# Performance work log

Measured on AMD Instinct MI355X. Metric: run time of the kernel, lower is better.

The kernel has to match this reference:

```python
import jax, jax.numpy as jnp
import numpy as np

# dims: batch, seq, d_model, heads, blocks
B, S, D, H, L = 8, 2048, 128, 4, 2
DK = D // H
SCALE = 1.0 / float(DK) ** 0.5
EPS = 1e-8  # LayerNorm eps from the torch module
NEG = -1000000000.0


def _ln(x, g, b):
    m = jnp.mean(x, axis=-1, keepdims=True)
    v = jnp.mean((x - m) ** 2, axis=-1, keepdims=True)
    return (x - m) * jax.lax.rsqrt(v + EPS) * g + b


def setup_inputs() -> dict:
    key = jax.random.key(0)
    ks = jax.random.split(key, 16)
    s = 0.02
    return {
        "log_seqs": jax.random.randint(ks[0], (B, S), 0, 50000),
        "seqs": jax.random.normal(ks[1], (B, S, D), dtype=jnp.float32),
        "Wqkv": jax.random.normal(ks[2], (L, 3, D, D), dtype=jnp.float32) * s,
        "bqkv": jnp.zeros((L, 3, D), dtype=jnp.float32),
        "ln1_g": jnp.ones((L, D), dtype=jnp.float32),
        "ln1_b": jnp.zeros((L, D), dtype=jnp.float32),
        "ln2_g": jnp.ones((L, D), dtype=jnp.float32),
        "ln2_b": jnp.zeros((L, D), dtype=jnp.float32),
        "W1": jax.random.normal(ks[3], (L, D, D), dtype=jnp.float32) * s,
        "b1": jnp.zeros((L, D), dtype=jnp.float32),
        "W2": jax.random.normal(ks[4], (L, D, D), dtype=jnp.float32) * s,
        "b2": jnp.zeros((L, D), dtype=jnp.float32),
        "lng": jnp.ones((D,), dtype=jnp.float32),
        "lnb": jnp.zeros((D,), dtype=jnp.float32),
    }


def reference(log_seqs, seqs, Wqkv, bqkv, ln1_g, ln1_b, ln2_g, ln2_b,
              W1, b1, W2, b2, lng, lnb):
    # dropout layers are identity at eval time
    keep = (log_seqs != 0)[:, :, None].astype(seqs.dtype)  # [B,S,1]
    causal = jnp.tril(jnp.ones((S, S), dtype=bool))        # [S,S]
    maskf = causal.astype(seqs.dtype)
    x = seqs * keep
    for i in range(L):
        q_in = _ln(x, ln1_g[i], ln1_b[i])                  # Q is layernormed; K,V are not
        q = (q_in @ Wqkv[i, 0] + bqkv[i, 0]).reshape(B, S, H, DK)
        k = (x    @ Wqkv[i, 1] + bqkv[i, 1]).reshape(B, S, H, DK)
        v = (x    @ Wqkv[i, 2] + bqkv[i, 2]).reshape(B, S, H, DK)
        scores = jnp.einsum('bqhd,bkhd->bhqk', q, k) * SCALE
        scores = jnp.where(causal, scores, NEG)
        p = jax.nn.softmax(scores, axis=-1) * maskf        # extra mask multiply as in source
        attn = jnp.einsum('bhqk,bkhd->bqhd', p, v).reshape(B, S, D)
        x = q_in + attn                                    # residual from layernormed Q
        x = _ln(x, ln2_g[i], ln2_b[i])
        x = x + jnp.maximum(x @ W1[i] + b1[i], 0.0) @ W2[i] + b2[i]  # kernel-1 convs == linears
        x = x * keep
    x = _ln(x, lng, lnb) * keep
    return x
```

## Files before the change

### kernel.cpp

```cpp
#include <hip/hip_runtime.h>
#include <hip/hip_bf16.h>
#include <math.h>

#define BB 8
#define SS 2048
#define DM 128
#define NH 4
#define DKH 32
#define NL 2
#define NROWS (BB*SS)

typedef __attribute__((ext_vector_type(8))) short bf16x8;
typedef __attribute__((ext_vector_type(4))) short short4v;
typedef __attribute__((ext_vector_type(4))) float f32x4;

#define SCALE 0.17677669529663687f
#define LNEPS 1e-8f

#define KSTR 40
#define VSTR 72
#define PSTR 72
#define WTS 136

__device__ __forceinline__ short f2bf(float f) {
    union { __hip_bfloat16 h; short s; } u;
    u.h = __float2bfloat16(f);
    return u.s;
}

__global__ __launch_bounds__(256) void mask_kernel(const float* __restrict__ seqs,
                                                   const int* __restrict__ logs,
                                                   float* __restrict__ x) {
    int i4 = blockIdx.x * 256 + threadIdx.x;
    int row = i4 >> 5;
    float4 v = ((const float4*)seqs)[i4];
    float km = (logs[row] != 0) ? 1.0f : 0.0f;
    v.x *= km; v.y *= km; v.z *= km; v.w *= km;
    ((float4*)x)[i4] = v;
}

template<bool HAS_RES, bool HAS_KEEP>
__global__ __launch_bounds__(256) void ln_kernel(const float* __restrict__ X,
                                                 const float* __restrict__ R,
                                                 const float* __restrict__ g,
                                                 const float* __restrict__ bb,
                                                 const int* __restrict__ logs,
                                                 float* __restrict__ Y) {
    int wave = threadIdx.x >> 6, lane = threadIdx.x & 63;
    int row = blockIdx.x * 4 + wave;
    const float2* xp = (const float2*)(X + (size_t)row * DM);
    float2 xv = xp[lane];
    if (HAS_RES) {
        float2 rv = ((const float2*)(R + (size_t)row * DM))[lane];
        xv.x += rv.x; xv.y += rv.y;
    }
    float s = xv.x + xv.y;
    #pragma unroll
    for (int off = 1; off < 64; off <<= 1) s += __shfl_xor(s, off);
    float mean = s * (1.0f / DM);
    float dx = xv.x - mean, dy = xv.y - mean;
    float vs = dx * dx + dy * dy;
    #pragma unroll
    for (int off = 1; off < 64; off <<= 1) vs += __shfl_xor(vs, off);
    float rstd = rsqrtf(vs * (1.0f / DM) + LNEPS);
    float2 gv = ((const float2*)g)[lane];
    float2 bv = ((const float2*)bb)[lane];
    float y0 = dx * rstd * gv.x + bv.x;
    float y1 = dy * rstd * gv.y + bv.y;
    if (HAS_KEEP) {
        float km = (logs[row] != 0) ? 1.0f : 0.0f;
        y0 *= km; y1 *= km;
    }
    float2 o; o.x = y0; o.y = y1;
    ((float2*)(Y + (size_t)row * DM))[lane] = o;
}

template<bool RELU, bool HAS_RES, bool HAS_KEEP, bool OUT_BF16>
__device__ __forceinline__ void gemm_core(const float* __restrict__ A,
                                          const float* __restrict__ W,
                                          const float* __restrict__ bias,
                                          const float* __restrict__ R,
                                          const int* __restrict__ logs,
                                          void* __restrict__ C) {
    __shared__ short Wt[128 * WTS];
    int tid = threadIdx.x;
    int rbase = blockIdx.x * 64;

    {
        int jj = tid & 127;
        int kh = tid >> 7;
        #pragma unroll
        for (int i = 0; i < 8; i++) {
            int k8 = kh + i * 2;
            bf16x8 wv;
            #pragma unroll
            for (int kk = 0; kk < 8; kk++)
                wv[kk] = f2bf(W[(k8 * 8 + kk) * DM + jj]);
            *(bf16x8*)&Wt[jj * WTS + k8 * 8] = wv;
        }
    }
    __syncthreads();

    int w = tid >> 6, l = tid & 63;
    int c = l & 15, g = l >> 4;
    int row_a = rbase + w * 16 + c;

    f32x4 acc[8];
    #pragma unroll
    for (int n = 0; n < 8; n++) acc[n] = (f32x4){0.f, 0.f, 0.f, 0.f};

    #pragma unroll
    for (int k0 = 0; k0 < 128; k0 += 32) {
        const float* ap = A + (size_t)row_a * DM + k0 + g * 8;
        float4 a0 = *(const float4*)ap;
        float4 a1 = *(const float4*)(ap + 4);
        bf16x8 af = { f2bf(a0.x), f2bf(a0.y), f2bf(a0.z), f2bf(a0.w),
                      f2bf(a1.x), f2bf(a1.y), f2bf(a1.z), f2bf(a1.w) };
        __builtin_amdgcn_s_setprio(1);
        #pragma unroll
        for (int n = 0; n < 8; n++) {
            bf16x8 bf = *(bf16x8*)&Wt[(n * 16 + c) * WTS + k0 + g * 8];
            acc[n] = __builtin_amdgcn_mfma_f32_16x16x32_bf16(af, bf, acc[n], 0, 0, 0);
        }
        __builtin_amdgcn_s_setprio(0);
    }

    int row0 = rbase + w * 16 + g * 4;
    float km[4];
    if (HAS_KEEP) {
        #pragma unroll
        for (int r = 0; r < 4; r++) km[r] = (logs[row0 + r] != 0) ? 1.0f : 0.0f;
    }
    #pragma unroll
    for (int n = 0; n < 8; n++) {
        float bv = bias[n * 16 + c];
        #pragma unroll
        for (int r = 0; r < 4; r++) {
            float o = acc[n][r] + bv;
            if (RELU) o = fmaxf(o, 0.0f);
            if (HAS_RES) o += R[(size_t)(row0 + r) * DM + n * 16 + c];
            if (HAS_KEEP) o *= km[r];
            size_t idx = (size_t)(row0 + r) * DM + n * 16 + c;
            if (OUT_BF16) ((short*)C)[idx] = f2bf(o);
            else ((float*)C)[idx] = o;
        }
    }
}

template<bool RELU, bool HAS_RES, bool HAS_KEEP, bool OUT_BF16>
__global__ __launch_bounds__(256) void gemm_mfma_kernel(const float* __restrict__ A,
                                                        const float* __restrict__ W,
                                                        const float* __restrict__ bias,
                                                        const float* __restrict__ R,
                                                        const int* __restrict__ logs,
                                                        void* __restrict__ C) {
    gemm_core<RELU, HAS_RES, HAS_KEEP, OUT_BF16>(A, W, bias, R, logs, C);
}

__global__ __launch_bounds__(256) void gemm_qkv_kernel(const float* __restrict__ qin,
                                                       const float* __restrict__ x,
                                                       const float* __restrict__ Wl,
                                                       const float* __restrict__ bl,
                                                       short* __restrict__ qkv) {
    int y = blockIdx.y;
    const float* A = (y == 0) ? qin : x;
    gemm_core<false, false, false, true>(A, Wl + (size_t)y * DM * DM, bl + y * DM,
                                         nullptr, nullptr,
                                         (void*)(qkv + (size_t)y * NROWS * DM));
}

__global__ __launch_bounds__(256) void attn_mfma_kernel(const short* __restrict__ Qg,
                                                        const short* __restrict__ Kg,
                                                        const short* __restrict__ Vg,
                                                        float* __restrict__ Og) {
    __shared__ short Ks[64 * KSTR];
    __shared__ short Vt[32 * VSTR];
    __shared__ short Pl[64 * PSTR];

    int tid = threadIdx.x;
    int qt = (gridDim.x - 1) - blockIdx.x;
    int h = blockIdx.y, b = blockIdx.z;
    int w = tid >> 6, l = tid & 63;
    int c = l & 15, g = l >> 4;

    int qbase = qt * 64;
    int qrow = qbase + w * 16 + c;
    int wqmin = qbase + w * 16;
    size_t bhoff = (size_t)b * SS * DM + (size_t)h * DKH;

    bf16x8 qf = *(const bf16x8*)(Qg + bhoff + (size_t)qrow * DM + g * 8);
    f32x4 acc[2] = { (f32x4){0,0,0,0}, (f32x4){0,0,0,0} };
    float mrun = -1e30f, lrun = 0.f;
    int ntiles = qt + 1;

    int kkey = tid >> 2, kpart = tid & 3;
    int vkey = tid & 63, vpart = tid >> 6;

    for (int kt = 0; kt < ntiles; kt++) {
        int kb = kt * 64;
        __syncthreads();
        bf16x8 kv8 = *(const bf16x8*)(Kg + bhoff + (size_t)(kb + kkey) * DM + kpart * 8);
        *(bf16x8*)&Ks[kkey * KSTR + kpart * 8] = kv8;
        bf16x8 vv8 = *(const bf16x8*)(Vg + bhoff + (size_t)(kb + vkey) * DM + vpart * 8);
        #pragma unroll
        for (int j = 0; j < 8; j++) Vt[(vpart * 8 + j) * VSTR + vkey] = vv8[j];
        __syncthreads();

        bf16x8 kf[4];
        #pragma unroll
        for (int t = 0; t < 4; t++)
            kf[t] = *(bf16x8*)&Ks[(t * 16 + c) * KSTR + g * 8];

        f32x4 z = {0.f, 0.f, 0.f, 0.f};
        f32x4 sc[4];
        __builtin_amdgcn_s_setprio(1);
        #pragma unroll
        for (int t = 0; t < 4; t++)
            sc[t] = __builtin_amdgcn_mfma_f32_16x16x32_bf16(kf[t], qf, z, 0, 0, 0);
        __builtin_amdgcn_s_setprio(0);

        float pv[16];
        float mx = -1e30f;
        if ((kb + 63) > wqmin) {
            #pragma unroll
            for (int t = 0; t < 4; t++)
                #pragma unroll
                for (int r = 0; r < 4; r++) {
                    int kg = kb + t * 16 + g * 4 + r;
                    float v2 = (kg <= qrow) ? sc[t][r] * SCALE : -1e30f;
                    pv[t * 4 + r] = v2;
                    mx = fmaxf(mx, v2);
                }
        } else {
            #pragma unroll
            for (int t = 0; t < 4; t++)
                #pragma unroll
                for (int r = 0; r < 4; r++) {
                    float v2 = sc[t][r] * SCALE;
                    pv[t * 4 + r] = v2;
                    mx = fmaxf(mx, v2);
                }
        }
        mx = fmaxf(mx, __shfl_xor(mx, 16));
        mx = fmaxf(mx, __shfl_xor(mx, 32));
        float mn = fmaxf(mrun, mx);
        float corr = __expf(mrun - mn);
        mrun = mn;
        float rs = 0.f;
        #pragma unroll
        for (int i = 0; i < 16; i++) {
            float p = __expf(pv[i] - mn);
            pv[i] = p;
            rs += p;
        }
        rs += __shfl_xor(rs, 16);
        rs += __shfl_xor(rs, 32);
        lrun = lrun * corr + rs;
        acc[0] *= corr;
        acc[1] *= corr;

        #pragma unroll
        for (int t = 0; t < 4; t++) {
            short4v p4 = { f2bf(pv[t * 4 + 0]), f2bf(pv[t * 4 + 1]),
                           f2bf(pv[t * 4 + 2]), f2bf(pv[t * 4 + 3]) };
            *(short4v*)&Pl[(w * 16 + c) * PSTR + t * 16 + g * 4] = p4;
        }
        bf16x8 va[2][2];
        #pragma unroll
        for (int t2 = 0; t2 < 2; t2++)
            #pragma unroll
            for (int kh = 0; kh < 2; kh++)
                va[t2][kh] = *(bf16x8*)&Vt[(t2 * 16 + c) * VSTR + kh * 32 + g * 8];
        bf16x8 pb[2];
        #pragma unroll
        for (int kh = 0; kh < 2; kh++)
            pb[kh] = *(bf16x8*)&Pl[(w * 16 + c) * PSTR + kh * 32 + g * 8];
        __builtin_amdgcn_s_setprio(1);
        #pragma unroll
        for (int kh = 0; kh < 2; kh++)
            #pragma unroll
            for (int t2 = 0; t2 < 2; t2++)
                acc[t2] = __builtin_amdgcn_mfma_f32_16x16x32_bf16(va[t2][kh], pb[kh], acc[t2], 0, 0, 0);
        __builtin_amdgcn_s_setprio(0);
    }
    float inv = 1.0f / lrun;
    #pragma unroll
    for (int t2 = 0; t2 < 2; t2++) {
        f32x4 ov = acc[t2] * inv;
        *(f32x4*)(Og + bhoff + (size_t)qrow * DM + t2 * 16 + g * 4) = ov;
    }
}

extern "C" void kernel_launch(void* const* d_in, const int* in_sizes, int n_in,
                              void* d_out, int out_size, void* d_ws, size_t ws_size,
                              hipStream_t stream) {
    const int*   logs = (const int*)d_in[0];
    const float* seqs = (const float*)d_in[1];
    const float* Wqkv = (const float*)d_in[2];
    const float* bqkv = (const float*)d_in[3];
    const float* ln1g = (const float*)d_in[4];
    const float* ln1b = (const float*)d_in[5];
    const float* ln2g = (const float*)d_in[6];
    const float* ln2b = (const float*)d_in[7];
    const float* W1   = (const float*)d_in[8];
    const float* b1   = (const float*)d_in[9];
    const float* W2   = (const float*)d_in[10];
    const float* b2   = (const float*)d_in[11];
    const float* lng  = (const float*)d_in[12];
    const float* lnb  = (const float*)d_in[13];
    float* out = (float*)d_out;
    float* ws  = (float*)d_ws;

    size_t ND = (size_t)NROWS * DM;
    float* x    = ws;
    float* qin  = x + ND;
    float* o    = qin + ND;
    float* hbuf = o + ND;
    short* qkv  = (short*)(hbuf + ND);
    short* q    = qkv;
    short* k    = qkv + ND;
    short* v    = qkv + 2 * ND;

    mask_kernel<<<(NROWS * DM) / 4 / 256, 256, 0, stream>>>(seqs, logs, x);

    for (int i = 0; i < NL; i++) {
        ln_kernel<false, false><<<NROWS / 4, 256, 0, stream>>>(x, nullptr, ln1g + i * DM, ln1b + i * DM, nullptr, qin);

        gemm_qkv_kernel<<<dim3(NROWS / 64, 3), 256, 0, stream>>>(qin, x,
            Wqkv + (size_t)i * 3 * DM * DM, bqkv + (size_t)i * 3 * DM, qkv);

        attn_mfma_kernel<<<dim3(SS / 64, NH, BB), 256, 0, stream>>>(q, k, v, o);

        ln_kernel<true, false><<<NROWS / 4, 256, 0, stream>>>(qin, o, ln2g + i * DM, ln2b + i * DM, nullptr, x);

        gemm_mfma_kernel<true, false, false, false><<<NROWS / 64, 256, 0, stream>>>(x, W1 + (size_t)i * DM * DM, b1 + i * DM, nullptr, nullptr, (void*)hbuf);

        gemm_mfma_kernel<false, true, true, false><<<NROWS / 64, 256, 0, stream>>>(hbuf, W2 + (size_t)i * DM * DM, b2 + i * DM, x, logs, (void*)x);
    }

    ln_kernel<false, true><<<NROWS / 4, 256, 0, stream>>>(x, nullptr, lng, lnb, logs, out);
}
```

Before: 283.8 us.

## Pre-convert weights to swizzled bf16 image, prefetch K/V tiles, lazy softmax rescale

Adds a one-time kernel per call that converts all weight matrices to bf16 in a transposed, XOR-swizzled layout, so every GEMM block copies a ready-made image into shared memory instead of doing strided fp32 loads and per-element conversion. The attention kernel now register-prefetches the next K/V tile while the current one is in use. The online softmax skips the rescale of the running max unless the new maximum exceeds it by more than a threshold. This adds an extra launch and workspace, and the lazy rescale can grow exponentials up to e^8 before correction.

```diff
diff --git a/kernel.cpp b/kernel.cpp
--- a/kernel.cpp
+++ b/kernel.cpp
@@ -20,7 +20,6 @@
 #define KSTR 40
 #define VSTR 72
 #define PSTR 72
-#define WTS 136
 
 __device__ __forceinline__ short f2bf(float f) {
     union { __hip_bfloat16 h; short s; } u;
@@ -75,35 +74,53 @@
     ((float2*)(Y + (size_t)row * DM))[lane] = o;
 }
 
+__global__ __launch_bounds__(256) void prep_w_kernel(const float* __restrict__ Wqkv,
+                                                     const float* __restrict__ W1,
+                                                     const float* __restrict__ W2,
+                                                     short* __restrict__ wimg) {
+    __shared__ short tile[16 * 128];
+    int bid = blockIdx.x;
+    int m = bid >> 3, jg = bid & 7;
+    const float* src = (m < 6) ? (Wqkv + (size_t)m * 16384)
+                     : (m < 8) ? (W1 + (size_t)(m - 6) * 16384)
+                               : (W2 + (size_t)(m - 8) * 16384);
+    int tid = threadIdx.x;
+    #pragma unroll
+    for (int it = 0; it < 8; it++) {
+        int e = it * 256 + tid;
+        int jj = e & 15;
+        int k  = e >> 4;
+        float v = src[(size_t)k * DM + jg * 16 + jj];
+        tile[jj * 128 + (k ^ ((jj & 7) << 3))] = f2bf(v);
+    }
+    __syncthreads();
+    short* dst = wimg + (size_t)m * 16384 + jg * 2048;
+    *(bf16x8*)&dst[tid * 8] = *(bf16x8*)&tile[tid * 8];
+}
+
 template<bool RELU, bool HAS_RES, bool HAS_KEEP, bool OUT_BF16>
 __device__ __forceinline__ void gemm_core(const float* __restrict__ A,
-                                          const float* __restrict__ W,
+                                          const short* __restrict__ Wimg,
                                           const float* __restrict__ bias,
                                           const float* __restrict__ R,
                                           const int* __restrict__ logs,
                                           void* __restrict__ C) {
-    __shared__ short Wt[128 * WTS];
+    __shared__ short Wt[128 * 128];
     int tid = threadIdx.x;
     int rbase = blockIdx.x * 64;
 
-    {
-        int jj = tid & 127;
-        int kh = tid >> 7;
-        #pragma unroll
-        for (int i = 0; i < 8; i++) {
-            int k8 = kh + i * 2;
-            bf16x8 wv;
-            #pragma unroll
-            for (int kk = 0; kk < 8; kk++)
-                wv[kk] = f2bf(W[(k8 * 8 + kk) * DM + jj]);
-            *(bf16x8*)&Wt[jj * WTS + k8 * 8] = wv;
-        }
+    #pragma unroll
+    for (int it = 0; it < 8; it++) {
+        int e = it * 256 + tid;
+        bf16x8 wv = *(const bf16x8*)(Wimg + (size_t)e * 8);
+        *(bf16x8*)&Wt[e * 8] = wv;
     }
     __syncthreads();
 
     int w = tid >> 6, l = tid & 63;
     int c = l & 15, g = l >> 4;
     int row_a = rbase + w * 16 + c;
+    int c7s = (c & 7) << 3;
 
     f32x4 acc[8];
     #pragma unroll
@@ -119,7 +136,8 @@
         __builtin_amdgcn_s_setprio(1);
         #pragma unroll
         for (int n = 0; n < 8; n++) {
-            bf16x8 bf = *(bf16x8*)&Wt[(n * 16 + c) * WTS + k0 + g * 8];
+            int row = n * 16 + c;
+            bf16x8 bf = *(bf16x8*)&Wt[row * 128 + ((k0 + g * 8) ^ c7s)];
             acc[n] = __builtin_amdgcn_mfma_f32_16x16x32_bf16(af, bf, acc[n], 0, 0, 0);
         }
         __builtin_amdgcn_s_setprio(0);
@@ -149,22 +167,22 @@
 
 template<bool RELU, bool HAS_RES, bool HAS_KEEP, bool OUT_BF16>
 __global__ __launch_bounds__(256) void gemm_mfma_kernel(const float* __restrict__ A,
-                                                        const float* __restrict__ W,
+                                                        const short* __restrict__ Wimg,
                                                         const float* __restrict__ bias,
                                                         const float* __restrict__ R,
                                                         const int* __restrict__ logs,
                                                         void* __restrict__ C) {
-    gemm_core<RELU, HAS_RES, HAS_KEEP, OUT_BF16>(A, W, bias, R, logs, C);
+    gemm_core<RELU, HAS_RES, HAS_KEEP, OUT_BF16>(A, Wimg, bias, R, logs, C);
 }
 
 __global__ __launch_bounds__(256) void gemm_qkv_kernel(const float* __restrict__ qin,
                                                        const float* __restrict__ x,
-                                                       const float* __restrict__ Wl,
+                                                       const short* __restrict__ Wimgl,
                                                        const float* __restrict__ bl,
                                                        short* __restrict__ qkv) {
     int y = blockIdx.y;
     const float* A = (y == 0) ? qin : x;
-    gemm_core<false, false, false, true>(A, Wl + (size_t)y * DM * DM, bl + y * DM,
+    gemm_core<false, false, false, true>(A, Wimgl + (size_t)y * 16384, bl + y * DM,
                                          nullptr, nullptr,
                                          (void*)(qkv + (size_t)y * NROWS * DM));
 }
@@ -196,14 +214,20 @@
     int kkey = tid >> 2, kpart = tid & 3;
     int vkey = tid & 63, vpart = tid >> 6;
 
+    bf16x8 kv8 = *(const bf16x8*)(Kg + bhoff + (size_t)kkey * DM + kpart * 8);
+    bf16x8 vv8 = *(const bf16x8*)(Vg + bhoff + (size_t)vkey * DM + vpart * 8);
+
     for (int kt = 0; kt < ntiles; kt++) {
         int kb = kt * 64;
         __syncthreads();
-        bf16x8 kv8 = *(const bf16x8*)(Kg + bhoff + (size_t)(kb + kkey) * DM + kpart * 8);
         *(bf16x8*)&Ks[kkey * KSTR + kpart * 8] = kv8;
-        bf16x8 vv8 = *(const bf16x8*)(Vg + bhoff + (size_t)(kb + vkey) * DM + vpart * 8);
         #pragma unroll
         for (int j = 0; j < 8; j++) Vt[(vpart * 8 + j) * VSTR + vkey] = vv8[j];
+        if (kt + 1 < ntiles) {
+            int kb2 = kb + 64;
+            kv8 = *(const bf16x8*)(Kg + bhoff + (size_t)(kb2 + kkey) * DM + kpart * 8);
+            vv8 = *(const bf16x8*)(Vg + bhoff + (size_t)(kb2 + vkey) * DM + vpart * 8);
+        }
         __syncthreads();
 
         bf16x8 kf[4];
@@ -243,21 +267,24 @@
         }
         mx = fmaxf(mx, __shfl_xor(mx, 16));
         mx = fmaxf(mx, __shfl_xor(mx, 32));
-        float mn = fmaxf(mrun, mx);
-        float corr = __expf(mrun - mn);
-        mrun = mn;
+        if (!__all(mx - mrun <= 8.0f)) {
+            float mn = fmaxf(mrun, mx);
+            float corr = __expf(mrun - mn);
+            lrun *= corr;
+            acc[0] *= corr;
+            acc[1] *= corr;
+            mrun = mn;
+        }
         float rs = 0.f;
         #pragma unroll
         for (int i = 0; i < 16; i++) {
-            float p = __expf(pv[i] - mn);
+            float p = __expf(pv[i] - mrun);
             pv[i] = p;
             rs += p;
         }
         rs += __shfl_xor(rs, 16);
         rs += __shfl_xor(rs, 32);
-        lrun = lrun * corr + rs;
-        acc[0] *= corr;
-        acc[1] *= corr;
+        lrun += rs;
 
         #pragma unroll
         for (int t = 0; t < 4; t++) {
@@ -320,22 +347,24 @@
     short* q    = qkv;
     short* k    = qkv + ND;
     short* v    = qkv + 2 * ND;
-
+    short* wimg = qkv + 3 * ND;
+
+    prep_w_kernel<<<80, 256, 0, stream>>>(Wqkv, W1, W2, wimg);
     mask_kernel<<<(NROWS * DM) / 4 / 256, 256, 0, stream>>>(seqs, logs, x);
 
     for (int i = 0; i < NL; i++) {
         ln_kernel<false, false><<<NROWS / 4, 256, 0, stream>>>(x, nullptr, ln1g + i * DM, ln1b + i * DM, nullptr, qin);
 
         gemm_qkv_kernel<<<dim3(NROWS / 64, 3), 256, 0, stream>>>(qin, x,
-            Wqkv + (size_t)i * 3 * DM * DM, bqkv + (size_t)i * 3 * DM, qkv);
+            wimg + (size_t)(i * 3) * 16384, bqkv + (size_t)i * 3 * DM, qkv);
 
         attn_mfma_kernel<<<dim3(SS / 64, NH, BB), 256, 0, stream>>>(q, k, v, o);
 
         ln_kernel<true, false><<<NROWS / 4, 256, 0, stream>>>(qin, o, ln2g + i * DM, ln2b + i * DM, nullptr, x);
 
-        gemm_mfma_kernel<true, false, false, false><<<NROWS / 64, 256, 0, stream>>>(x, W1 + (size_t)i * DM * DM, b1 + i * DM, nullptr, nullptr, (void*)hbuf);
-
-        gemm_mfma_kernel<false, true, true, false><<<NROWS / 64, 256, 0, stream>>>(hbuf, W2 + (size_t)i * DM * DM, b2 + i * DM, x, logs, (void*)x);
+        gemm_mfma_kernel<true, false, false, false><<<NROWS / 64, 256, 0, stream>>>(x, wimg + (size_t)(6 + i) * 16384, b1 + i * DM, nullptr, nullptr, (void*)hbuf);
+
+        gemm_mfma_kernel<false, true, true, false><<<NROWS / 64, 256, 0, stream>>>(hbuf, wimg + (size_t)(8 + i) * 16384, b2 + i * DM, x, logs, (void*)x);
     }
 
     ln_kernel<false, true><<<NROWS / 4, 256, 0, stream>>>(x, nullptr, lng, lnb, logs, out);
```

Measured after the change: 275.9 us. 1.03x faster.
